# Kernel optimization log

Hardware: AMD Instinct MI355X
Metric: run time of the kernel (lower is better)

The kernel has to match this reference:

```python
import jax, jax.numpy as jnp
import numpy as np

HID = 1024; HEADS = 16; HD = 64; INTER = 4096; NLAYERS = 4
PATCH = 16; IMG_SIZE = 1024; MAXSIDE = IMG_SIZE // PATCH
THETA = 10000.0; EPS = 1e-5; SCALE = HD ** -0.5


def setup_inputs() -> dict:
    key = jax.random.key(0)
    ks = jax.random.split(key, 11)
    s = 0.02
    w = lambda k, shape: jax.random.normal(k, shape, jnp.float32) * s
    return {
        "img0": jax.random.normal(ks[0], (3, 512, 512), jnp.float32),
        "img1": jax.random.normal(ks[1], (3, 512, 256), jnp.float32),
        "conv_w": w(ks[2], (HID, 3, PATCH, PATCH)),
        "ln_pre_w": jnp.ones((HID,), jnp.float32),
        "attn_norm_w": jnp.ones((NLAYERS, HID), jnp.float32),
        "q_w": w(ks[3], (NLAYERS, HID, HID)),
        "k_w": w(ks[4], (NLAYERS, HID, HID)),
        "v_w": w(ks[5], (NLAYERS, HID, HID)),
        "o_w": w(ks[6], (NLAYERS, HID, HID)),
        "ffn_norm_w": jnp.ones((NLAYERS, HID), jnp.float32),
        "gate_w": w(ks[7], (NLAYERS, INTER, HID)),
        "up_w": w(ks[8], (NLAYERS, INTER, HID)),
        "down_w": w(ks[9], (NLAYERS, HID, INTER)),
    }


def _rms(x, wt):
    return x * jax.lax.rsqrt(jnp.mean(x * x, axis=-1, keepdims=True) + EPS) * wt


def _rot_half(x):
    return jnp.concatenate([-x[..., HD // 2:], x[..., :HD // 2]], axis=-1)


def reference(img0, img1, conv_w, ln_pre_w, attn_norm_w, q_w, k_w, v_w, o_w,
              ffn_norm_w, gate_w, up_w, down_w):
    dn = ('NCHW', 'OIHW', 'NCHW')
    grids, embeds = [], []
    for img in (img0, img1):
        p = jax.lax.conv_general_dilated(img[None], conv_w, (PATCH, PATCH),
                                         'VALID', dimension_numbers=dn)  # [1,HID,h,w]
        h, wd = p.shape[2], p.shape[3]
        grids.append((h, wd))
        embeds.append(p.reshape(1, HID, h * wd).transpose(0, 2, 1))
    x = jnp.concatenate(embeds, axis=1)  # [1, S, HID]
    S = x.shape[1]
    x = _rms(x, ln_pre_w)

    # meshgrid position ids: h*MAXSIDE + w per image
    pids = jnp.concatenate([
        (jnp.arange(h)[:, None] * MAXSIDE + jnp.arange(wd)[None, :]).reshape(-1)
        for h, wd in grids])
    # Pixtral 2D RoPE frequency table
    freqs = 1.0 / THETA ** (jnp.arange(0, HD, 2, dtype=jnp.float32) / HD)  # [HD/2]
    fh = jnp.outer(jnp.arange(MAXSIDE, dtype=jnp.float32), freqs[::2])   # [64, HD/4]
    fw = jnp.outer(jnp.arange(MAXSIDE, dtype=jnp.float32), freqs[1::2])  # [64, HD/4]
    inv = jnp.concatenate([
        jnp.broadcast_to(fh[:, None, :], (MAXSIDE, MAXSIDE, HD // 4)),
        jnp.broadcast_to(fw[None, :, :], (MAXSIDE, MAXSIDE, HD // 4))],
        axis=-1).reshape(-1, HD // 2)
    inv = jnp.concatenate([inv, inv], axis=-1)  # [MAXSIDE^2, HD]
    emb = inv[pids]                              # [S, HD]
    cos = jnp.cos(emb)[None, None]               # [1,1,S,HD]
    sin = jnp.sin(emb)[None, None]

    # block-diagonal additive mask (images don't attend across each other)
    neg = jnp.finfo(jnp.float32).min
    mask = jnp.full((S, S), neg, jnp.float32)
    off = 0
    for h, wd in grids:
        n = h * wd
        mask = mask.at[off:off + n, off:off + n].set(0.0)
        off += n

    def layer(xc, p):
        an, qw, kw, vw, ow, fn, gw, uw, dw = p
        hn = _rms(xc, an)
        heads = lambda y, wm: jnp.einsum('bsd,ed->bse', y, wm).reshape(
            1, S, HEADS, HD).transpose(0, 2, 1, 3)  # [1,H,S,D]
        q, k, v = heads(hn, qw), heads(hn, kw), heads(hn, vw)
        q = q * cos + _rot_half(q) * sin
        k = k * cos + _rot_half(k) * sin
        scores = jnp.einsum('bhqd,bhkd->bhqk', q, k) * SCALE + mask
        aw = jax.nn.softmax(scores.astype(jnp.float32), axis=-1).astype(xc.dtype)
        o = jnp.einsum('bhqk,bhkd->bhqd', aw, v).transpose(0, 2, 1, 3).reshape(1, S, HID)
        h2 = xc + jnp.einsum('bsd,ed->bse', o, ow)
        m = _rms(h2, fn)
        ff = jnp.einsum(
            'bsi,di->bsd',
            jax.nn.silu(jnp.einsum('bsd,id->bsi', m, gw)) * jnp.einsum('bsd,id->bsi', m, uw),
            dw)
        return h2 + ff, None

    out, _ = jax.lax.scan(layer, x, (attn_norm_w, q_w, k_w, v_w, o_w,
                                     ffn_norm_w, gate_w, up_w, down_w))
    return out
```

## Files before the change

### kernel.cpp

```cpp
#include <hip/hip_runtime.h>
#include <hip/hip_bf16.h>
#include <math.h>

#define S_TOT 1536
#define S0    1024
#define HID   1024
#define HEADS 16
#define HD    64
#define INTER 4096
#define NLAYERS 4
#define KCONV 768
#define EPSV  1e-5f
#define SCALEV 0.125f
#define QKS   2048

typedef __attribute__((ext_vector_type(8))) __bf16 bf16x8;
typedef __attribute__((ext_vector_type(8))) unsigned short u16x8;
typedef __attribute__((ext_vector_type(4))) float f32x4;
typedef __attribute__((address_space(1))) void gvoid;
typedef __attribute__((address_space(3))) void lvoid;

__device__ __forceinline__ ushort f2bf(float f) {
    union { float f; unsigned u; } v; v.f = f;
    unsigned u = v.u;
    return (ushort)((u + 0x7FFFu + ((u >> 16) & 1u)) >> 16);
}
__device__ __forceinline__ float bf2f(ushort b) {
    union { unsigned u; float f; } v; v.u = ((unsigned)b) << 16;
    return v.f;
}

template<int N> __device__ __forceinline__ void wait_vm() {
    if constexpr (N == 0)      asm volatile("s_waitcnt vmcnt(0)" ::: "memory");
    else if constexpr (N == 2) asm volatile("s_waitcnt vmcnt(2)" ::: "memory");
    else if constexpr (N == 4) asm volatile("s_waitcnt vmcnt(4)" ::: "memory");
    else if constexpr (N == 8) asm volatile("s_waitcnt vmcnt(8)" ::: "memory");
    else                       asm volatile("s_waitcnt vmcnt(0)" ::: "memory");
}

__global__ __launch_bounds__(256) void cvt_kernel(
    const float* __restrict__ src, ushort* __restrict__ dst, int n4)
{
    int i = blockIdx.x * 256 + threadIdx.x;
    if (i < n4) {
        float4 v = ((const float4*)src)[i];
        ushort4 o;
        o.x = f2bf(v.x); o.y = f2bf(v.y); o.z = f2bf(v.z); o.w = f2bf(v.w);
        ((ushort4*)dst)[i] = o;
    }
}

__global__ __launch_bounds__(256) void cvt_layer_kernel(
    const float* __restrict__ qw, const float* __restrict__ kw,
    const float* __restrict__ vw, const float* __restrict__ ow,
    const float* __restrict__ gw, const float* __restrict__ uw,
    const float* __restrict__ dw, ushort* __restrict__ dst)
{
    int i = blockIdx.x * 256 + threadIdx.x;
    int e = i << 2;
    const float* src; int off; size_t de;
    if      (e < (1  << 20)) { src = qw; off = e;             de = e; }
    else if (e < (2  << 20)) { src = kw; off = e - (1 << 20); de = e; }
    else if (e < (3  << 20)) { src = vw; off = e - (2 << 20); de = e; }
    else if (e < (4  << 20)) { src = ow; off = e - (3 << 20); de = e; }
    else if (e < (8  << 20)) {
        src = gw; off = e - (4 << 20);
        int chan = off >> 10, col = off & 1023;
        de = (size_t)(4 << 20) + (size_t)(((chan >> 4) << 5) + (chan & 15)) * 1024 + col;
    }
    else if (e < (12 << 20)) {
        src = uw; off = e - (8 << 20);
        int chan = off >> 10, col = off & 1023;
        de = (size_t)(4 << 20) + (size_t)(((chan >> 4) << 5) + 16 + (chan & 15)) * 1024 + col;
    }
    else                     { src = dw; off = e - (12 << 20); de = e; }
    float4 v = *(const float4*)(src + off);
    ushort4 o;
    o.x = f2bf(v.x); o.y = f2bf(v.y); o.z = f2bf(v.z); o.w = f2bf(v.w);
    *(ushort4*)(dst + de) = o;
}

__global__ __launch_bounds__(256) void im2col_kernel(
    const float* __restrict__ img0, const float* __restrict__ img1,
    ushort* __restrict__ P)
{
    int s = blockIdx.x;
    const float* img; int W, ph, pw;
    if (s < S0) { img = img0; W = 512; ph = s >> 5; pw = s & 31; }
    else { int t = s - S0; img = img1; W = 256; ph = t >> 4; pw = t & 15; }
    for (int k = threadIdx.x; k < KCONV; k += 256) {
        int c = k >> 8; int r = k & 255; int y = r >> 4; int x = r & 15;
        P[(size_t)s * KCONV + k] =
            f2bf(img[(size_t)c * 512 * W + (size_t)(ph * 16 + y) * W + (pw * 16 + x)]);
    }
}

#define STAGE_LAMBDA(NLA_, NLB_)                                                 \
    auto stage = [&](int b, int k0) {                                            \
        _Pragma("unroll")                                                        \
        for (int i_ = 0; i_ < NLA_; ++i_) {                                      \
            int idx = t + i_ * 256;                                              \
            int r_ = idx >> 2, c8_ = (idx & 3) << 3;                             \
            __builtin_amdgcn_global_load_lds(                                    \
                (gvoid*)(A + (size_t)(bm + r_) * K + k0 + c8_),                  \
                (lvoid*)(&As[b][idx * 8]), 16, 0, 0);                            \
        }                                                                        \
        _Pragma("unroll")                                                        \
        for (int i_ = 0; i_ < NLB_; ++i_) {                                      \
            int idx = t + i_ * 256;                                              \
            int r_ = idx >> 2, c8_ = (idx & 3) << 3;                             \
            __builtin_amdgcn_global_load_lds(                                    \
                (gvoid*)(B + (size_t)(bn + r_) * K + k0 + c8_),                  \
                (lvoid*)(&Bs[b][idx * 8]), 16, 0, 0);                            \
        }                                                                        \
    };

#define LOOP3B_HEAD(NL_, KBASE_)                                                 \
    stage(0, KBASE_); stage(1, KBASE_ + 32);                                     \
    int cbuf = 0, sbuf = 2;                                                      \
    for (int kt = 0; kt < NKT; ++kt) {                                           \
        if (kt + 1 < NKT) wait_vm<NL_>(); else wait_vm<0>();                     \
        __builtin_amdgcn_sched_barrier(0);                                       \
        __builtin_amdgcn_s_barrier();                                            \
        __builtin_amdgcn_sched_barrier(0);                                       \
        if (kt + 2 < NKT) {                                                      \
            stage(sbuf, KBASE_ + ((kt + 2) << 5));                               \
            sbuf = (sbuf == 2) ? 0 : sbuf + 1;                                   \
        }

#define LOOP3B_TAIL                                                              \
        cbuf = (cbuf == 2) ? 0 : cbuf + 1;                                       \
    }

template<int BM, int BN, bool OUT_BF16>
__global__ __launch_bounds__(256) void gemm3b(
    const ushort* __restrict__ A, const ushort* __restrict__ B,
    void* __restrict__ Cout, int M, int N, int K)
{
    constexpr int WMT = BM / 32, WNT = BN / 32;
    constexpr int NLA = (BM * 32) / (8 * 256);
    constexpr int NLB = (BN * 32) / (8 * 256);
    constexpr int NL  = NLA + NLB;
    __shared__ ushort As[3][BM * 32];
    __shared__ ushort Bs[3][BN * 32];
    const int t = threadIdx.x;
    const int bm = blockIdx.x * BM, bn = blockIdx.y * BN;
    const int wave = t >> 6, lane = t & 63;
    const int wm = (wave & 1) * (BM / 2), wn = (wave >> 1) * (BN / 2);
    const int frow = lane & 15, fq = lane >> 4;
    STAGE_LAMBDA(NLA, NLB)

    f32x4 acc[WMT][WNT];
    #pragma unroll
    for (int i = 0; i < WMT; ++i)
        #pragma unroll
        for (int j = 0; j < WNT; ++j) acc[i][j] = (f32x4){0.f, 0.f, 0.f, 0.f};

    const int NKT = K >> 5;
    LOOP3B_HEAD(NL, 0)
        bf16x8 af[WMT], bfr[WNT];
        #pragma unroll
        for (int i = 0; i < WMT; ++i)
            af[i] = *(const bf16x8*)(&As[cbuf][(wm + 16 * i + frow) * 32 + fq * 8]);
        #pragma unroll
        for (int j = 0; j < WNT; ++j)
            bfr[j] = *(const bf16x8*)(&Bs[cbuf][(wn + 16 * j + frow) * 32 + fq * 8]);
        __builtin_amdgcn_s_setprio(1);
        #pragma unroll
        for (int i = 0; i < WMT; ++i)
            #pragma unroll
            for (int j = 0; j < WNT; ++j)
                acc[i][j] = __builtin_amdgcn_mfma_f32_16x16x32_bf16(
                    af[i], bfr[j], acc[i][j], 0, 0, 0);
        __builtin_amdgcn_s_setprio(0);
    LOOP3B_TAIL
    #pragma unroll
    for (int i = 0; i < WMT; ++i) {
        #pragma unroll
        for (int j = 0; j < WNT; ++j) {
            #pragma unroll
            for (int r = 0; r < 4; ++r) {
                int row = bm + wm + 16 * i + fq * 4 + r;
                int col = bn + wn + 16 * j + frow;
                float vv = acc[i][j][r];
                if (OUT_BF16) ((ushort*)Cout)[(size_t)row * N + col] = f2bf(vv);
                else          ((float*)Cout)[(size_t)row * N + col] = vv;
            }
        }
    }
}

__global__ __launch_bounds__(256) void gemm3b_qkv(
    const ushort* __restrict__ A, const ushort* __restrict__ B,
    ushort* __restrict__ qkb, ushort* __restrict__ vT,
    const float* __restrict__ cs, const float* __restrict__ sn, int K)
{
    constexpr int BM = 128, BN = 128;
    __shared__ ushort As[3][BM * 32];
    __shared__ ushort Bs[3][BN * 32];
    const int t = threadIdx.x;
    const int bm = blockIdx.x * BM, bn = blockIdx.y * BN;
    const int wave = t >> 6, lane = t & 63;
    const int wm = (wave & 1) * 64, wn = (wave >> 1) * 64;
    const int frow = lane & 15, fq = lane >> 4;
    STAGE_LAMBDA(2, 2)

    f32x4 acc[4][4];
    #pragma unroll
    for (int i = 0; i < 4; ++i)
        #pragma unroll
        for (int j = 0; j < 4; ++j) acc[i][j] = (f32x4){0.f, 0.f, 0.f, 0.f};

    const int NKT = K >> 5;
    LOOP3B_HEAD(4, 0)
        bf16x8 af[4], bfr[4];
        #pragma unroll
        for (int i = 0; i < 4; ++i)
            af[i] = *(const bf16x8*)(&As[cbuf][(wm + 16 * i + frow) * 32 + fq * 8]);
        #pragma unroll
        for (int j = 0; j < 4; ++j)
            bfr[j] = *(const bf16x8*)(&Bs[cbuf][(wn + 16 * j + frow) * 32 + fq * 8]);
        __builtin_amdgcn_s_setprio(1);
        #pragma unroll
        for (int i = 0; i < 4; ++i)
            #pragma unroll
            for (int j = 0; j < 4; ++j)
                acc[i][j] = __builtin_amdgcn_mfma_f32_16x16x32_bf16(
                    af[i], bfr[j], acc[i][j], 0, 0, 0);
        __builtin_amdgcn_s_setprio(0);
    LOOP3B_TAIL
    const int colbase = bn + wn;
    const int part = colbase >> 10;
    if (part < 2) {
        #pragma unroll
        for (int i = 0; i < 4; ++i) {
            #pragma unroll
            for (int r = 0; r < 4; ++r) {
                int row = bm + wm + 16 * i + fq * 4 + r;
                float cv0 = cs[row * 32 + frow],      sv0 = sn[row * 32 + frow];
                float cv1 = cs[row * 32 + 16 + frow], sv1 = sn[row * 32 + 16 + frow];
                float xa0 = acc[i][0][r], xa1 = acc[i][1][r];
                float xb0 = acc[i][2][r], xb1 = acc[i][3][r];
                ushort* dst = qkb + (size_t)row * QKS + (part << 10) + (colbase & 1023) + frow;
                dst[0]  = f2bf(xa0 * cv0 - xb0 * sv0);
                dst[16] = f2bf(xa1 * cv1 - xb1 * sv1);
                dst[32] = f2bf(xb0 * cv0 + xa0 * sv0);
                dst[48] = f2bf(xb1 * cv1 + xa1 * sv1);
            }
        }
    } else {
        const int hh = (colbase - 2048) >> 6;
        #pragma unroll
        for (int i = 0; i < 4; ++i) {
            int row = bm + wm + 16 * i + (fq << 2);
            #pragma unroll
            for (int j = 0; j < 4; ++j) {
                int d = 16 * j + frow;
                ushort4 o4;
                o4.x = f2bf(acc[i][j][0]); o4.y = f2bf(acc[i][j][1]);
                o4.z = f2bf(acc[i][j][2]); o4.w = f2bf(acc[i][j][3]);
                *(ushort4*)(vT + ((size_t)hh * HD + d) * S_TOT + row) = o4;
            }
        }
    }
}

__global__ __launch_bounds__(256) void gemm3b_gu(
    const ushort* __restrict__ A, const ushort* __restrict__ B,
    ushort* __restrict__ gb, int K)
{
    constexpr int BM = 128, BN = 128;
    __shared__ ushort As[3][BM * 32];
    __shared__ ushort Bs[3][BN * 32];
    const int t = threadIdx.x;
    const int bm = blockIdx.x * BM, bn = blockIdx.y * BN;
    const int wave = t >> 6, lane = t & 63;
    const int wm = (wave & 1) * 64, wn = (wave >> 1) * 64;
    const int frow = lane & 15, fq = lane >> 4;
    STAGE_LAMBDA(2, 2)

    f32x4 acc[4][4];
    #pragma unroll
    for (int i = 0; i < 4; ++i)
        #pragma unroll
        for (int j = 0; j < 4; ++j) acc[i][j] = (f32x4){0.f, 0.f, 0.f, 0.f};

    const int NKT = K >> 5;
    LOOP3B_HEAD(4, 0)
        bf16x8 af[4], bfr[4];
        #pragma unroll
        for (int i = 0; i < 4; ++i)
            af[i] = *(const bf16x8*)(&As[cbuf][(wm + 16 * i + frow) * 32 + fq * 8]);
        #pragma unroll
        for (int j = 0; j < 4; ++j)
            bfr[j] = *(const bf16x8*)(&Bs[cbuf][(wn + 16 * j + frow) * 32 + fq * 8]);
        __builtin_amdgcn_s_setprio(1);
        #pragma unroll
        for (int i = 0; i < 4; ++i)
            #pragma unroll
            for (int j = 0; j < 4; ++j)
                acc[i][j] = __builtin_amdgcn_mfma_f32_16x16x32_bf16(
                    af[i], bfr[j], acc[i][j], 0, 0, 0);
        __builtin_amdgcn_s_setprio(0);
    LOOP3B_TAIL
    #pragma unroll
    for (int i = 0; i < 4; ++i) {
        #pragma unroll
        for (int p = 0; p < 2; ++p) {
            int chan = ((bn + wn) >> 1) + p * 16 + frow;
            #pragma unroll
            for (int r = 0; r < 4; ++r) {
                int row = bm + wm + 16 * i + fq * 4 + r;
                float g = acc[i][2 * p][r], u = acc[i][2 * p + 1][r];
                float sg = 1.f / (1.f + __expf(-g));
                gb[(size_t)row * INTER + chan] = f2bf(g * sg * u);
            }
        }
    }
}

template<int SPLITK>
__global__ __launch_bounds__(256) void gemm3b_sk(
    const ushort* __restrict__ A, const ushort* __restrict__ B,
    float* __restrict__ P, int M, int N, int K)
{
    constexpr int BM = 128, BN = 128;
    __shared__ ushort As[3][BM * 32];
    __shared__ ushort Bs[3][BN * 32];
    const int t = threadIdx.x;
    const int bm = blockIdx.x * BM, bn = blockIdx.y * BN;
    const int kc = K / SPLITK;
    const int kb = blockIdx.z * kc;
    const int wave = t >> 6, lane = t & 63;
    const int wm = (wave & 1) * 64, wn = (wave >> 1) * 64;
    const int frow = lane & 15, fq = lane >> 4;
    STAGE_LAMBDA(2, 2)

    f32x4 acc[4][4];
    #pragma unroll
    for (int i = 0; i < 4; ++i)
        #pragma unroll
        for (int j = 0; j < 4; ++j) acc[i][j] = (f32x4){0.f, 0.f, 0.f, 0.f};

    const int NKT = kc >> 5;
    LOOP3B_HEAD(4, kb)
        bf16x8 af[4], bfr[4];
        #pragma unroll
        for (int i = 0; i < 4; ++i)
            af[i] = *(const bf16x8*)(&As[cbuf][(wm + 16 * i + frow) * 32 + fq * 8]);
        #pragma unroll
        for (int j = 0; j < 4; ++j)
            bfr[j] = *(const bf16x8*)(&Bs[cbuf][(wn + 16 * j + frow) * 32 + fq * 8]);
        __builtin_amdgcn_s_setprio(1);
        #pragma unroll
        for (int i = 0; i < 4; ++i)
            #pragma unroll
            for (int j = 0; j < 4; ++j)
                acc[i][j] = __builtin_amdgcn_mfma_f32_16x16x32_bf16(
                    af[i], bfr[j], acc[i][j], 0, 0, 0);
        __builtin_amdgcn_s_setprio(0);
    LOOP3B_TAIL
    float* Pz = P + (size_t)blockIdx.z * M * N;
    #pragma unroll
    for (int i = 0; i < 4; ++i) {
        #pragma unroll
        for (int j = 0; j < 4; ++j) {
            #pragma unroll
            for (int r = 0; r < 4; ++r) {
                int row = bm + wm + 16 * i + fq * 4 + r;
                int col = bn + wn + 16 * j + frow;
                Pz[(size_t)row * N + col] = acc[i][j][r];
            }
        }
    }
}

__global__ __launch_bounds__(256) void reduce4_kernel(
    const float* __restrict__ P, float* __restrict__ x, int n4)
{
    int i = blockIdx.x * 256 + threadIdx.x;
    if (i >= n4) return;
    const int n = n4 << 2;
    float4 a  = ((const float4*)x)[i];
    float4 p0 = ((const float4*)P)[i];
    float4 p1 = ((const float4*)(P + (size_t)n))[i];
    float4 p2 = ((const float4*)(P + (size_t)2 * n))[i];
    float4 p3 = ((const float4*)(P + (size_t)3 * n))[i];
    a.x += p0.x + p1.x + p2.x + p3.x;
    a.y += p0.y + p1.y + p2.y + p3.y;
    a.z += p0.z + p1.z + p2.z + p3.z;
    a.w += p0.w + p1.w + p2.w + p3.w;
    ((float4*)x)[i] = a;
}

__global__ __launch_bounds__(256) void reduce_rms_bf_kernel(
    const float* __restrict__ P, float* __restrict__ x,
    const float* __restrict__ w, ushort* __restrict__ out)
{
    int row = blockIdx.x, t = threadIdx.x;
    size_t off = (size_t)row * HID + t * 4;
    float4 a = *(const float4*)(x + off);
    #pragma unroll
    for (int z = 0; z < 4; ++z) {
        float4 p = *(const float4*)(P + (size_t)z * S_TOT * HID + off);
        a.x += p.x; a.y += p.y; a.z += p.z; a.w += p.w;
    }
    *(float4*)(x + off) = a;
    float ss = a.x * a.x + a.y * a.y + a.z * a.z + a.w * a.w;
    #pragma unroll
    for (int o = 32; o > 0; o >>= 1) ss += __shfl_down(ss, o, 64);
    __shared__ float red[4];
    int wid = t >> 6;
    if ((t & 63) == 0) red[wid] = ss;
    __syncthreads();
    if (t == 0)
        red[0] = rsqrtf((red[0] + red[1] + red[2] + red[3]) / HID + EPSV);
    __syncthreads();
    float rs = red[0];
    const float* wp = w + t * 4;
    ushort4 o4;
    o4.x = f2bf(a.x * rs * wp[0]); o4.y = f2bf(a.y * rs * wp[1]);
    o4.z = f2bf(a.z * rs * wp[2]); o4.w = f2bf(a.w * rs * wp[3]);
    *(ushort4*)(out + off) = o4;
}

__global__ __launch_bounds__(256) void rms_kernel(
    const float* __restrict__ in, const float* __restrict__ w,
    float* __restrict__ out)
{
    int row = blockIdx.x;
    const float* xr = in + (size_t)row * HID;
    float ss = 0.f;
    for (int i = threadIdx.x; i < HID; i += 256) { float v = xr[i]; ss += v * v; }
    #pragma unroll
    for (int off = 32; off > 0; off >>= 1) ss += __shfl_down(ss, off, 64);
    __shared__ float red[4];
    int wid = threadIdx.x >> 6;
    if ((threadIdx.x & 63) == 0) red[wid] = ss;
    __syncthreads();
    if (threadIdx.x == 0)
        red[0] = rsqrtf((red[0] + red[1] + red[2] + red[3]) / HID + EPSV);
    __syncthreads();
    float rs = red[0];
    for (int i = threadIdx.x; i < HID; i += 256)
        out[(size_t)row * HID + i] = xr[i] * rs * w[i];
}

__global__ __launch_bounds__(256) void rms_bf_kernel(
    const float* __restrict__ in, const float* __restrict__ w,
    ushort* __restrict__ out)
{
    int row = blockIdx.x;
    const float* xr = in + (size_t)row * HID;
    float ss = 0.f;
    for (int i = threadIdx.x; i < HID; i += 256) { float v = xr[i]; ss += v * v; }
    #pragma unroll
    for (int off = 32; off > 0; off >>= 1) ss += __shfl_down(ss, off, 64);
    __shared__ float red[4];
    int wid = threadIdx.x >> 6;
    if ((threadIdx.x & 63) == 0) red[wid] = ss;
    __syncthreads();
    if (threadIdx.x == 0)
        red[0] = rsqrtf((red[0] + red[1] + red[2] + red[3]) / HID + EPSV);
    __syncthreads();
    float rs = red[0];
    for (int i = threadIdx.x; i < HID; i += 256)
        out[(size_t)row * HID + i] = f2bf(xr[i] * rs * w[i]);
}

__global__ void rope_tab_kernel(float* __restrict__ cs, float* __restrict__ sn)
{
    int s = blockIdx.x; int j = threadIdx.x;
    int h, w;
    if (s < S0) { h = s >> 5; w = s & 31; }
    else { int t = s - S0; h = t >> 4; w = t & 15; }
    float f;
    if (j < 16) f = (float)h * powf(10000.f, -(4.f * j) / 64.f);
    else        f = (float)w * powf(10000.f, -(4.f * (j - 16) + 2.f) / 64.f);
    cs[s * 32 + j] = cosf(f);
    sn[s * 32 + j] = sinf(f);
}

__global__ __launch_bounds__(256) void flash_mfma_kernel(
    const ushort* __restrict__ qkb, const ushort* __restrict__ vT,
    ushort* __restrict__ o)
{
    __shared__ ushort Ks[64 * 72];
    __shared__ ushort Vt[64 * 72];
    __shared__ ushort Ps[4 * 16 * 72];
    int tile = blockIdx.x;
    int hh = blockIdx.y;
    int segStart, q0, nkt;
    if (tile < 16) { segStart = 0; q0 = tile << 6; nkt = 16; }
    else { segStart = S0; q0 = S0 + ((tile - 16) << 6); nkt = 8; }
    const int t = threadIdx.x;
    const int wave = t >> 6, lane = t & 63;
    const int c = lane & 15, fq = lane >> 4;
    const int wq = wave << 4;
    ushort* Pw = Ps + wave * 16 * 72;

    bf16x8 qf[2];
    #pragma unroll
    for (int ks = 0; ks < 2; ++ks)
        qf[ks] = *(const bf16x8*)(qkb + (size_t)(q0 + wq + c) * QKS + hh * HD + ks * 32 + fq * 8);

    float m_i[4], l_i[4];
    f32x4 accO[4];
    #pragma unroll
    for (int r = 0; r < 4; ++r) { m_i[r] = -1e30f; l_i[r] = 0.f; }
    #pragma unroll
    for (int nt = 0; nt < 4; ++nt) accO[nt] = (f32x4){0.f, 0.f, 0.f, 0.f};

    for (int kt = 0; kt < nkt; ++kt) {
        int kbase = segStart + (kt << 6);
        __syncthreads();
        #pragma unroll
        for (int i = 0; i < 2; ++i) {
            int u = t + (i << 8);
            int r = u >> 3, c8 = (u & 7) << 3;
            u16x8 kv = *(const u16x8*)(qkb + (size_t)(kbase + r) * QKS + 1024 + hh * HD + c8);
            *(u16x8*)(Ks + r * 72 + c8) = kv;
            u16x8 vv = *(const u16x8*)(vT + ((size_t)hh * HD + r) * S_TOT + kbase + c8);
            *(u16x8*)(Vt + r * 72 + c8) = vv;
        }
        __syncthreads();

        f32x4 acc[4];
        #pragma unroll
        for (int nt = 0; nt < 4; ++nt) acc[nt] = (f32x4){0.f, 0.f, 0.f, 0.f};
        #pragma unroll
        for (int ks = 0; ks < 2; ++ks) {
            #pragma unroll
            for (int nt = 0; nt < 4; ++nt) {
                bf16x8 bfr = *(const bf16x8*)(Ks + (nt * 16 + c) * 72 + ks * 32 + fq * 8);
                acc[nt] = __builtin_amdgcn_mfma_f32_16x16x32_bf16(qf[ks], bfr, acc[nt], 0, 0, 0);
            }
        }

        #pragma unroll
        for (int r = 0; r < 4; ++r) {
            float s0v = acc[0][r] * SCALEV, s1v = acc[1][r] * SCALEV;
            float s2v = acc[2][r] * SCALEV, s3v = acc[3][r] * SCALEV;
            float rm = fmaxf(fmaxf(s0v, s1v), fmaxf(s2v, s3v));
            #pragma unroll
            for (int msk = 1; msk < 16; msk <<= 1)
                rm = fmaxf(rm, __shfl_xor(rm, msk, 64));
            float mn = fmaxf(m_i[r], rm);
            float al = __expf(m_i[r] - mn);
            float p0 = __expf(s0v - mn), p1 = __expf(s1v - mn);
            float p2 = __expf(s2v - mn), p3 = __expf(s3v - mn);
            float rs = p0 + p1 + p2 + p3;
            #pragma unroll
            for (int msk = 1; msk < 16; msk <<= 1)
                rs += __shfl_xor(rs, msk, 64);
            l_i[r] = l_i[r] * al + rs;
            m_i[r] = mn;
            #pragma unroll
            for (int nt = 0; nt < 4; ++nt) accO[nt][r] *= al;
            int qrow = (fq << 2) + r;
            Pw[qrow * 72 + 0  + c] = f2bf(p0);
            Pw[qrow * 72 + 16 + c] = f2bf(p1);
            Pw[qrow * 72 + 32 + c] = f2bf(p2);
            Pw[qrow * 72 + 48 + c] = f2bf(p3);
        }

        #pragma unroll
        for (int ks = 0; ks < 2; ++ks) {
            bf16x8 pa = *(const bf16x8*)(Pw + c * 72 + ks * 32 + fq * 8);
            #pragma unroll
            for (int nt = 0; nt < 4; ++nt) {
                bf16x8 bv = *(const bf16x8*)(Vt + (nt * 16 + c) * 72 + ks * 32 + fq * 8);
                accO[nt] = __builtin_amdgcn_mfma_f32_16x16x32_bf16(pa, bv, accO[nt], 0, 0, 0);
            }
        }
    }

    #pragma unroll
    for (int r = 0; r < 4; ++r) {
        float inv = 1.f / l_i[r];
        int row = q0 + wq + (fq << 2) + r;
        #pragma unroll
        for (int nt = 0; nt < 4; ++nt)
            o[(size_t)row * HID + hh * HD + nt * 16 + c] = f2bf(accO[nt][r] * inv);
    }
}

__global__ __launch_bounds__(256) void copy_kernel(
    const float* __restrict__ src, float* __restrict__ dst, int n)
{
    int i = blockIdx.x * 256 + threadIdx.x;
    if (i < n) dst[i] = src[i];
}

extern "C" void kernel_launch(void* const* d_in, const int* in_sizes, int n_in,
                              void* d_out, int out_size, void* d_ws, size_t ws_size,
                              hipStream_t stream)
{
    const float* img0        = (const float*)d_in[0];
    const float* img1        = (const float*)d_in[1];
    const float* conv_w      = (const float*)d_in[2];
    const float* ln_pre_w    = (const float*)d_in[3];
    const float* attn_norm_w = (const float*)d_in[4];
    const float* q_w         = (const float*)d_in[5];
    const float* k_w         = (const float*)d_in[6];
    const float* v_w         = (const float*)d_in[7];
    const float* o_w         = (const float*)d_in[8];
    const float* ffn_norm_w  = (const float*)d_in[9];
    const float* gate_w      = (const float*)d_in[10];
    const float* up_w        = (const float*)d_in[11];
    const float* down_w      = (const float*)d_in[12];

    char* p = (char*)d_ws;
    float* x    = (float*)p;   p += (size_t)1572864 * 4;
    float* cs   = (float*)p;   p += (size_t)49152 * 4;
    float* sn   = (float*)p;   p += (size_t)49152 * 4;
    ushort* qkb = (ushort*)p;  p += (size_t)3145728 * 2;
    ushort* vTb = (ushort*)p;  p += (size_t)1572864 * 2;
    ushort* hnb = (ushort*)p;  p += (size_t)1572864 * 2;
    ushort* obb = (ushort*)p;  p += (size_t)1572864 * 2;
    ushort* gb  = (ushort*)p;  p += (size_t)6291456 * 2;
    float* skP  = (float*)p;   p += (size_t)6291456 * 4;
    ushort* Pb  = (ushort*)p;  p += (size_t)1179648 * 2;
    ushort* cvb = (ushort*)p;  p += (size_t)786432 * 2;
    ushort* wbuf= (ushort*)p;  p += (size_t)16777216 * 2;

    ushort* wqkv = wbuf;
    ushort* wo   = wbuf + 3145728;
    ushort* wgu  = wbuf + 4194304;
    ushort* wdn  = wbuf + 12582912;

    dim3 blk(256);

    cvt_kernel<<<768, blk, 0, stream>>>(conv_w, cvb, 786432 / 4);
    im2col_kernel<<<S_TOT, blk, 0, stream>>>(img0, img1, Pb);
    gemm3b<64, 64, false><<<dim3(24, 16), blk, 0, stream>>>(
        Pb, cvb, x, S_TOT, HID, KCONV);
    rms_kernel<<<S_TOT, blk, 0, stream>>>(x, ln_pre_w, x);
    rope_tab_kernel<<<S_TOT, 32, 0, stream>>>(cs, sn);

    for (int l = 0; l < NLAYERS; ++l) {
        cvt_layer_kernel<<<16384, blk, 0, stream>>>(
            q_w + (size_t)l * 1048576, k_w + (size_t)l * 1048576,
            v_w + (size_t)l * 1048576, o_w + (size_t)l * 1048576,
            gate_w + (size_t)l * 4194304, up_w + (size_t)l * 4194304,
            down_w + (size_t)l * 4194304, wbuf);

        rms_bf_kernel<<<S_TOT, blk, 0, stream>>>(x, attn_norm_w + (size_t)l * HID, hnb);
        gemm3b_qkv<<<dim3(12, 24), blk, 0, stream>>>(
            hnb, wqkv, qkb, vTb, cs, sn, HID);
        flash_mfma_kernel<<<dim3(24, HEADS), blk, 0, stream>>>(qkb, vTb, obb);
        gemm3b_sk<4><<<dim3(12, 8, 4), blk, 0, stream>>>(
            obb, wo, skP, S_TOT, HID, HID);
        reduce_rms_bf_kernel<<<S_TOT, blk, 0, stream>>>(
            skP, x, ffn_norm_w + (size_t)l * HID, hnb);
        gemm3b_gu<<<dim3(12, 64), blk, 0, stream>>>(hnb, wgu, gb, HID);
        gemm3b_sk<4><<<dim3(12, 8, 4), blk, 0, stream>>>(
            gb, wdn, skP, S_TOT, HID, INTER);
        reduce4_kernel<<<1536, blk, 0, stream>>>(skP, x, S_TOT * HID / 4);
    }
    copy_kernel<<<(S_TOT * HID) / 256, blk, 0, stream>>>(x, (float*)d_out, S_TOT * HID);
}
```

Before: 918.8 us.

## XOR-swizzle GEMM LDS tiles and fuse next-layer RMSNorm into residual reduce

Applies an XOR swizzle to the 16-byte chunk index inside each 32-element LDS row, both when staging from global memory and when reading MFMA fragments. The aim is to cut LDS bank conflicts in all GEMM variants. Separately, the down-projection split-K reduce is merged with the following layer's attention RMSNorm through reduce_rms_bf_kernel, which drops one kernel launch and one pass over the activations per layer. The swizzle makes the global load addresses less contiguous within a row.

```diff
diff --git a/kernel.cpp b/kernel.cpp
--- a/kernel.cpp
+++ b/kernel.cpp
@@ -100,17 +100,19 @@
         _Pragma("unroll")                                                        \
         for (int i_ = 0; i_ < NLA_; ++i_) {                                      \
             int idx = t + i_ * 256;                                              \
-            int r_ = idx >> 2, c8_ = (idx & 3) << 3;                             \
+            int r_ = idx >> 2, sp_ = idx & 3;                                    \
+            int lc_ = sp_ ^ (r_ & 3);                                            \
             __builtin_amdgcn_global_load_lds(                                    \
-                (gvoid*)(A + (size_t)(bm + r_) * K + k0 + c8_),                  \
+                (gvoid*)(A + (size_t)(bm + r_) * K + k0 + (lc_ << 3)),           \
                 (lvoid*)(&As[b][idx * 8]), 16, 0, 0);                            \
         }                                                                        \
         _Pragma("unroll")                                                        \
         for (int i_ = 0; i_ < NLB_; ++i_) {                                      \
             int idx = t + i_ * 256;                                              \
-            int r_ = idx >> 2, c8_ = (idx & 3) << 3;                             \
+            int r_ = idx >> 2, sp_ = idx & 3;                                    \
+            int lc_ = sp_ ^ (r_ & 3);                                            \
             __builtin_amdgcn_global_load_lds(                                    \
-                (gvoid*)(B + (size_t)(bn + r_) * K + k0 + c8_),                  \
+                (gvoid*)(B + (size_t)(bn + r_) * K + k0 + (lc_ << 3)),           \
                 (lvoid*)(&Bs[b][idx * 8]), 16, 0, 0);                            \
         }                                                                        \
     };
@@ -131,6 +133,11 @@
 #define LOOP3B_TAIL                                                              \
         cbuf = (cbuf == 2) ? 0 : cbuf + 1;                                       \
     }
+
+#define LDS_A(i_) (*(const bf16x8*)(&As[cbuf][((wm + 16 * (i_) + frow) << 5) + \
+                     ((fq ^ ((wm + 16 * (i_) + frow) & 3)) << 3)]))
+#define LDS_B(j_) (*(const bf16x8*)(&Bs[cbuf][((wn + 16 * (j_) + frow) << 5) + \
+                     ((fq ^ ((wn + 16 * (j_) + frow) & 3)) << 3)]))
 
 template<int BM, int BN, bool OUT_BF16>
 __global__ __launch_bounds__(256) void gemm3b(
@@ -160,11 +167,9 @@
     LOOP3B_HEAD(NL, 0)
         bf16x8 af[WMT], bfr[WNT];
         #pragma unroll
-        for (int i = 0; i < WMT; ++i)
-            af[i] = *(const bf16x8*)(&As[cbuf][(wm + 16 * i + frow) * 32 + fq * 8]);
-        #pragma unroll
-        for (int j = 0; j < WNT; ++j)
-            bfr[j] = *(const bf16x8*)(&Bs[cbuf][(wn + 16 * j + frow) * 32 + fq * 8]);
+        for (int i = 0; i < WMT; ++i) af[i] = LDS_A(i);
+        #pragma unroll
+        for (int j = 0; j < WNT; ++j) bfr[j] = LDS_B(j);
         __builtin_amdgcn_s_setprio(1);
         #pragma unroll
         for (int i = 0; i < WMT; ++i)
@@ -215,11 +220,9 @@
     LOOP3B_HEAD(4, 0)
         bf16x8 af[4], bfr[4];
         #pragma unroll
-        for (int i = 0; i < 4; ++i)
-            af[i] = *(const bf16x8*)(&As[cbuf][(wm + 16 * i + frow) * 32 + fq * 8]);
-        #pragma unroll
-        for (int j = 0; j < 4; ++j)
-            bfr[j] = *(const bf16x8*)(&Bs[cbuf][(wn + 16 * j + frow) * 32 + fq * 8]);
+        for (int i = 0; i < 4; ++i) af[i] = LDS_A(i);
+        #pragma unroll
+        for (int j = 0; j < 4; ++j) bfr[j] = LDS_B(j);
         __builtin_amdgcn_s_setprio(1);
         #pragma unroll
         for (int i = 0; i < 4; ++i)
@@ -289,11 +292,9 @@
     LOOP3B_HEAD(4, 0)
         bf16x8 af[4], bfr[4];
         #pragma unroll
-        for (int i = 0; i < 4; ++i)
-            af[i] = *(const bf16x8*)(&As[cbuf][(wm + 16 * i + frow) * 32 + fq * 8]);
-        #pragma unroll
-        for (int j = 0; j < 4; ++j)
-            bfr[j] = *(const bf16x8*)(&Bs[cbuf][(wn + 16 * j + frow) * 32 + fq * 8]);
+        for (int i = 0; i < 4; ++i) af[i] = LDS_A(i);
+        #pragma unroll
+        for (int j = 0; j < 4; ++j) bfr[j] = LDS_B(j);
         __builtin_amdgcn_s_setprio(1);
         #pragma unroll
         for (int i = 0; i < 4; ++i)
@@ -346,11 +347,9 @@
     LOOP3B_HEAD(4, kb)
         bf16x8 af[4], bfr[4];
         #pragma unroll
-        for (int i = 0; i < 4; ++i)
-            af[i] = *(const bf16x8*)(&As[cbuf][(wm + 16 * i + frow) * 32 + fq * 8]);
-        #pragma unroll
-        for (int j = 0; j < 4; ++j)
-            bfr[j] = *(const bf16x8*)(&Bs[cbuf][(wn + 16 * j + frow) * 32 + fq * 8]);
+        for (int i = 0; i < 4; ++i) af[i] = LDS_A(i);
+        #pragma unroll
+        for (int j = 0; j < 4; ++j) bfr[j] = LDS_B(j);
         __builtin_amdgcn_s_setprio(1);
         #pragma unroll
         for (int i = 0; i < 4; ++i)
@@ -637,6 +636,7 @@
         Pb, cvb, x, S_TOT, HID, KCONV);
     rms_kernel<<<S_TOT, blk, 0, stream>>>(x, ln_pre_w, x);
     rope_tab_kernel<<<S_TOT, 32, 0, stream>>>(cs, sn);
+    rms_bf_kernel<<<S_TOT, blk, 0, stream>>>(x, attn_norm_w, hnb);
 
     for (int l = 0; l < NLAYERS; ++l) {
         cvt_layer_kernel<<<16384, blk, 0, stream>>>(
@@ -645,7 +645,6 @@
             gate_w + (size_t)l * 4194304, up_w + (size_t)l * 4194304,
             down_w + (size_t)l * 4194304, wbuf);
 
-        rms_bf_kernel<<<S_TOT, blk, 0, stream>>>(x, attn_norm_w + (size_t)l * HID, hnb);
         gemm3b_qkv<<<dim3(12, 24), blk, 0, stream>>>(
             hnb, wqkv, qkb, vTb, cs, sn, HID);
         flash_mfma_kernel<<<dim3(24, HEADS), blk, 0, stream>>>(qkb, vTb, obb);
@@ -656,7 +655,11 @@
         gemm3b_gu<<<dim3(12, 64), blk, 0, stream>>>(hnb, wgu, gb, HID);
         gemm3b_sk<4><<<dim3(12, 8, 4), blk, 0, stream>>>(
             gb, wdn, skP, S_TOT, HID, INTER);
-        reduce4_kernel<<<1536, blk, 0, stream>>>(skP, x, S_TOT * HID / 4);
+        if (l + 1 < NLAYERS)
+            reduce_rms_bf_kernel<<<S_TOT, blk, 0, stream>>>(
+                skP, x, attn_norm_w + (size_t)(l + 1) * HID, hnb);
+        else
+            reduce4_kernel<<<1536, blk, 0, stream>>>(skP, x, S_TOT * HID / 4);
     }
     copy_kernel<<<(S_TOT * HID) / 256, blk, 0, stream>>>(x, (float*)d_out, S_TOT * HID);
 }
```

Result: no change. 902.8 us (-1.7%).
